# Kernel tuning notes

Hardware: AMD Instinct MI355X
Metric: run time of the kernel (lower is better)

## Reference

```python
import jax, jax.numpy as jnp
import numpy as np

BLANK = 1   # Offsets.GO
NEG = -1e30  # effective -inf that stays finite under logaddexp


def setup_inputs() -> dict:
    key = jax.random.key(0)
    k1, k2, k3, k4 = jax.random.split(key, 4)
    T, B, V, S = 1000, 64, 512, 100
    logits = jax.random.normal(k1, (T, B, V), dtype=jnp.float32)
    log_prob = jax.nn.log_softmax(logits, axis=-1)  # ctc_loss expects log-probs
    input_lengths = jax.random.randint(k2, (B,), T // 2, T + 1, dtype=jnp.int32)
    # target tokens avoid PAD(0)/GO(1,blank)/EOS(2), matching the masked_select semantics
    targets = jax.random.randint(k3, (B, S), 3, V, dtype=jnp.int32)
    target_lengths = jax.random.randint(k4, (B,), S // 2, S + 1, dtype=jnp.int32)
    return {"log_prob": log_prob, "input_lengths": input_lengths,
            "targets": targets, "target_lengths": target_lengths}


def _ctc_loss_sum(log_prob, input_lengths, targets, target_lengths):
    # log_prob: (T, B, V) log-softmax outputs; targets: (B, S) padded labels
    T, B, V = log_prob.shape
    S = targets.shape[1]
    Se = 2 * S + 1  # extended label sequence: blank-interleaved

    ext = jnp.full((B, Se), BLANK, dtype=targets.dtype).at[:, 1::2].set(targets)
    pos = jnp.arange(Se)
    ext_len = 2 * target_lengths + 1                      # (B,)
    valid = pos[None, :] < ext_len[:, None]               # (B, Se)
    ext_m2 = jnp.pad(ext[:, :-2], ((0, 0), (2, 0)), constant_values=BLANK)
    allow_skip = (ext != BLANK) & (ext != ext_m2) & (pos[None, :] >= 2)

    # emit[t, b, s] = log_prob[t, b, ext[b, s]]  -> (T, B, Se)
    emit = jnp.take_along_axis(log_prob, jnp.broadcast_to(ext[None], (T, B, Se)), axis=2)

    # alpha init at t=0
    alpha = jnp.full((B, Se), NEG, dtype=log_prob.dtype)
    alpha = alpha.at[:, 0].set(emit[0, :, 0])
    alpha = alpha.at[:, 1].set(jnp.where(target_lengths > 0, emit[0, :, 1], NEG))
    alpha = jnp.where(valid, alpha, NEG)

    def step(alpha, xt):
        emit_t, t = xt
        a1 = alpha
        a2 = jnp.pad(alpha[:, :-1], ((0, 0), (1, 0)), constant_values=NEG)
        a3 = jnp.where(allow_skip,
                       jnp.pad(alpha[:, :-2], ((0, 0), (2, 0)), constant_values=NEG),
                       NEG)
        new = jnp.logaddexp(jnp.logaddexp(a1, a2), a3) + emit_t
        new = jnp.where(valid, new, NEG)
        # freeze alpha once past each sample's input length
        alpha = jnp.where((t < input_lengths)[:, None], new, alpha)
        return alpha, None

    alpha, _ = jax.lax.scan(step, alpha, (emit[1:], jnp.arange(1, T)))

    last = 2 * target_lengths  # index of trailing blank in extended sequence
    a_last = jnp.take_along_axis(alpha, last[:, None], axis=1)[:, 0]
    a_prev = jnp.take_along_axis(alpha, jnp.maximum(last - 1, 0)[:, None], axis=1)[:, 0]
    loglik = jnp.logaddexp(a_last, a_prev)
    loss = -loglik
    # zero_infinity=True: infeasible alignments contribute 0
    loss = jnp.where(loglik < 0.5 * NEG, 0.0, loss)
    return jnp.sum(loss)  # reduction='sum'


def reference(log_prob, input_lengths, targets, target_lengths):
    return _ctc_loss_sum(log_prob, input_lengths, targets, target_lengths)
```

## Files before the change

kernel.cpp:

```cpp
#include <hip/hip_runtime.h>


#define NEGF (-1e30f)

constexpr int CT_T  = 1000;
constexpr int CT_B  = 64;
constexpr int CT_V  = 512;
constexpr int CT_S  = 100;
constexpr int CT_Se = 201;
constexpr float LOG2E = 1.4426950408889634f;
constexpr float LN2   = 0.6931471805599453f;
constexpr float SHIFT = 5.0f;

#if __has_builtin(__builtin_amdgcn_exp2f) && __has_builtin(__builtin_amdgcn_logf)
__device__ __forceinline__ float fexp2(float x) { return __builtin_amdgcn_exp2f(x); }
__device__ __forceinline__ float flog2(float x) { return __builtin_amdgcn_logf(x); }
__device__ __forceinline__ float frcp(float x)  { return __builtin_amdgcn_rcpf(x); }
#else
__device__ __forceinline__ float fexp2(float x) { return exp2f(x); }
__device__ __forceinline__ float flog2(float x) { return log2f(x); }
__device__ __forceinline__ float frcp(float x)  { return 1.0f / x; }
#endif

__device__ __forceinline__ float lae2_b2(float x, float y) {
    float m = fmaxf(x, y);
    float d = fminf(x, y) - m;
    return m + flog2(1.0f + fexp2(d));
}
__device__ __forceinline__ float lae3_b2(float x, float y, float z) {
    float m = fmaxf(fmaxf(x, y), z);
    float s = fexp2(x - m) + fexp2(y - m) + fexp2(z - m);
    return m + flog2(s);
}

__device__ __forceinline__ float wave_shr1(float x) {
    return __int_as_float(__builtin_amdgcn_update_dpp(
        0, __float_as_int(x), 0x138, 0xf, 0xf, true));
}
__device__ __forceinline__ float wave_max_nonneg(float x) {
#define DPPMAX(ctrl) x = fmaxf(x, __int_as_float(__builtin_amdgcn_update_dpp( \
        0, __float_as_int(x), ctrl, 0xf, 0xf, true)))
    DPPMAX(0x111); DPPMAX(0x112); DPPMAX(0x114); DPPMAX(0x118);
    DPPMAX(0x142); DPPMAX(0x143);
#undef DPPMAX
    return __int_as_float(__builtin_amdgcn_readlane(__float_as_int(x), 63));
}

typedef const __attribute__((address_space(1))) unsigned int* as1_uint_ptr;
typedef __attribute__((address_space(3))) unsigned int* as3_uint_ptr;
__device__ __forceinline__ void gld16(const void* g, void* l) {
    __builtin_amdgcn_global_load_lds((as1_uint_ptr)g, (as3_uint_ptr)l, 16, 0, 0);
}

__global__ __launch_bounds__(256, 1) void ctc_alpha(
    const float* __restrict__ logp,
    const int*   __restrict__ in_len,
    const int*   __restrict__ tgt,
    const int*   __restrict__ tgt_len,
    float*       __restrict__ loss_ws)
{
    __shared__ float ldsr[4][8][CT_V];

    const int b    = blockIdx.x;
    const int tid  = threadIdx.x;
    const int wv   = tid >> 6;
    const int lane = tid & 63;
    const int Tin  = in_len[b];
    const int Lt   = tgt_len[b];
    const int lim  = 2 * Lt + 1;
    const int* tg  = tgt + b * CT_S;

    const int Kf = (Tin - 1) / 8;
    const int K  = (Tin - 1 + 7) / 8;

    const int s0 = 4 * lane, s1 = s0 + 1, s3 = s0 + 3;
    const int i1 = min((s1 - 1) >> 1, CT_S - 1);
    const int i3 = min((s3 - 1) >> 1, CT_S - 1);
    const int c1 = tg[i1];
    const int c3 = tg[i3];
    const float sk1 = ((s1 >= 3) && (s1 < CT_Se) && (c1 != tg[max(i1 - 1, 0)])) ? 1.f : 0.f;
    const float sk3 = ((s3 >= 3) && (s3 < CT_Se) && (c3 != tg[max(i3 - 1, 0)])) ? 1.f : 0.f;
    const float m0 = (s0     < lim) ? 1.f : 0.f;
    const float m1 = (s0 + 1 < lim) ? 1.f : 0.f;
    const float m2 = (s0 + 2 < lim) ? 1.f : 0.f;
    const float m3 = (s0 + 3 < lim) ? 1.f : 0.f;

    float a0 = 0.f, a1 = 0.f, a2 = 0.f, a3 = 0.f, pa3 = 0.f;
    if (tid == 0) {
        const float* r0 = logp + (size_t)b * CT_V;
        a0 = fexp2(fmaf(r0[1], LOG2E, SHIFT));
        if (Lt > 0) a1 = fexp2(fmaf(r0[c1], LOG2E, SHIFT));
    }
    float rs = 0.f;

    auto issue = [&](int k, int buf) {
        const int tb = 1 + 8 * k;
        #pragma unroll
        for (int i = 0; i < 8; ++i) {
            const int t = min(tb + i, CT_T - 1);
            const char* g = (const char*)(logp + ((size_t)t * CT_B + b) * CT_V)
                          + (size_t)lane * 16;
            gld16(g,        &ldsr[buf][i][0]);
            gld16(g + 1024, &ldsr[buf][i][256]);
        }
    };

    auto renorm = [&]() {
        float lm = wave_max_nonneg(fmaxf(fmaxf(a0, a1), fmaxf(a2, a3)));
        if (lm > 0.f) {
            float sc = frcp(lm);
            rs += flog2(lm);
            a0 *= sc; a1 *= sc; a2 *= sc; a3 *= sc;
            pa3 = wave_shr1(a3);
        }
    };

    auto run8 = [&](int buf, int tb, bool guard) {
        unsigned base = (unsigned)(size_t)(&ldsr[buf][0][0]);
        unsigned ab = base + 4u * 1;
        unsigned a1a = base + 4u * (unsigned)c1;
        unsigned a3a = base + 4u * (unsigned)c3;
        float g0,g1,g2,g3,g4,g5,g6,g7,g8,g9,g10,g11,
              g12,g13,g14,g15,g16,g17,g18,g19,g20,g21,g22,g23;
        asm volatile(
            "ds_read_b32 %0,  %24 offset:0\n\t"
            "ds_read_b32 %1,  %25 offset:0\n\t"
            "ds_read_b32 %2,  %26 offset:0\n\t"
            "ds_read_b32 %3,  %24 offset:2048\n\t"
            "ds_read_b32 %4,  %25 offset:2048\n\t"
            "ds_read_b32 %5,  %26 offset:2048\n\t"
            "ds_read_b32 %6,  %24 offset:4096\n\t"
            "ds_read_b32 %7,  %25 offset:4096\n\t"
            "ds_read_b32 %8,  %26 offset:4096\n\t"
            "ds_read_b32 %9,  %24 offset:6144\n\t"
            "ds_read_b32 %10, %25 offset:6144\n\t"
            "ds_read_b32 %11, %26 offset:6144\n\t"
            "ds_read_b32 %12, %24 offset:8192\n\t"
            "ds_read_b32 %13, %25 offset:8192\n\t"
            "ds_read_b32 %14, %26 offset:8192\n\t"
            "ds_read_b32 %15, %24 offset:10240\n\t"
            "ds_read_b32 %16, %25 offset:10240\n\t"
            "ds_read_b32 %17, %26 offset:10240\n\t"
            "ds_read_b32 %18, %24 offset:12288\n\t"
            "ds_read_b32 %19, %25 offset:12288\n\t"
            "ds_read_b32 %20, %26 offset:12288\n\t"
            "ds_read_b32 %21, %24 offset:14336\n\t"
            "ds_read_b32 %22, %25 offset:14336\n\t"
            "ds_read_b32 %23, %26 offset:14336\n\t"
            "s_waitcnt lgkmcnt(0)"
            : "=&v"(g0), "=&v"(g1), "=&v"(g2), "=&v"(g3), "=&v"(g4), "=&v"(g5),
              "=&v"(g6), "=&v"(g7), "=&v"(g8), "=&v"(g9), "=&v"(g10), "=&v"(g11),
              "=&v"(g12), "=&v"(g13), "=&v"(g14), "=&v"(g15), "=&v"(g16), "=&v"(g17),
              "=&v"(g18), "=&v"(g19), "=&v"(g20), "=&v"(g21), "=&v"(g22), "=&v"(g23)
            : "v"(ab), "v"(a1a), "v"(a3a));

        float eb[8], e1[8], e3[8];
        float gb[24] = {g0,g1,g2,g3,g4,g5,g6,g7,g8,g9,g10,g11,
                        g12,g13,g14,g15,g16,g17,g18,g19,g20,g21,g22,g23};
        #pragma unroll
        for (int i = 0; i < 8; ++i) {
            eb[i] = fexp2(fmaf(gb[3 * i],     LOG2E, SHIFT));
            e1[i] = fexp2(fmaf(gb[3 * i + 1], LOG2E, SHIFT));
            e3[i] = fexp2(fmaf(gb[3 * i + 2], LOG2E, SHIFT));
        }
        #pragma unroll
        for (int i = 0; i < 8; ++i) {
            float ex = eb[i] * m0, ey = e1[i] * m1;
            float ez = eb[i] * m2, ew = e3[i] * m3;
            float n0 = (a0 + pa3) * ex;
            float n1 = fmaf(sk1, pa3, a1 + a0) * ey;
            float n2 = (a2 + a1) * ez;
            float n3 = fmaf(sk3, a1, a3 + a2) * ew;
            if (!guard || (tb + i < Tin)) { a0 = n0; a1 = n1; a2 = n2; a3 = n3; }
            pa3 = wave_shr1(a3);
        }
    };

    if (wv) {
        const int p = wv - 1;
        if (p < K) issue(p, p);
        if (p == 0)
            asm volatile("s_waitcnt vmcnt(0)" ::: "memory");
    }
    __builtin_amdgcn_s_barrier();

    for (int j = 0; j < K; ++j) {
        if (wv == 0) {
            if (j < Kf) { run8(j & 3, 0, false); if (j & 1) renorm(); }
            else        run8(j & 3, 1 + 8 * j, true);
        } else {
            const int p = wv - 1;
            if ((j % 3) == p && (j + 3) < K) issue(j + 3, (j + 3) & 3);
            if (((j + 1) % 3) == p && (j + 1) < K)
                asm volatile("s_waitcnt vmcnt(0)" ::: "memory");
        }
        __builtin_amdgcn_s_barrier();
    }

    if (wv) {
        asm volatile("s_waitcnt vmcnt(0)" ::: "memory");
        return;
    }

    const int last = 2 * Lt;
    const int prev = max(last - 1, 0);
    const int lr = last & 3, lidx = last >> 2;
    float av = (lr == 0) ? a0 : (lr == 1) ? a1 : (lr == 2) ? a2 : a3;
    float a_last = __shfl(av, lidx);
    const int pr = prev & 3, pidx = prev >> 2;
    float pv = (pr == 0) ? a0 : (pr == 1) ? a1 : (pr == 2) ? a2 : a3;
    float a_prev = __shfl(pv, pidx);

    float sum = a_last + a_prev;
    float loss = 0.f;
    if (sum > 0.f)
        loss = -(flog2(sum) + rs - SHIFT * (float)Tin) * LN2;
    if (lane == 0) loss_ws[b] = loss;
}

__global__ __launch_bounds__(64) void ctc_alpha_fb(
    const float* __restrict__ logp, const int* __restrict__ in_len,
    const int* __restrict__ tgt, const int* __restrict__ tgt_len,
    float* __restrict__ loss_ws)
{
    const int b = blockIdx.x, lane = threadIdx.x;
    const int Tin = in_len[b], Lt = tgt_len[b];
    const int ext_len = 2 * Lt + 1;
    const int* tg = tgt + b * CT_S;
    const int s0 = 4 * lane, s1 = s0 + 1, s3 = s0 + 3;
    const int i1 = min((s1 - 1) >> 1, CT_S - 1);
    const int i3 = min((s3 - 1) >> 1, CT_S - 1);
    const int c1 = tg[i1], c3 = tg[i3];
    const bool skip1 = (s1 >= 3) && (s1 < CT_Se) && (c1 != tg[max(i1 - 1, 0)]);
    const bool skip3 = (s3 >= 3) && (s3 < CT_Se) && (c3 != tg[max(i3 - 1, 0)]);
    const bool v0 = s0 < ext_len, v1 = s1 < ext_len;
    const bool v2 = (s0 + 2) < ext_len, v3 = s3 < ext_len;
    const float* row0 = logp + (long long)b * CT_V;
    const long long stride = (long long)CT_B * CT_V;
    float a0 = NEGF, a1 = NEGF, a2 = NEGF, a3 = NEGF;
    if (lane == 0) {
        a0 = row0[1] * LOG2E;
        if (ext_len > 1) a1 = row0[c1] * LOG2E;
    }
    float3 E0, E1, E2, E3;
    auto ld = [&](float3& e, int t) {
        int tt = min(t, CT_T - 1);
        const float* r = row0 + (long long)tt * stride;
        e.x = r[1] * LOG2E; e.y = r[c1] * LOG2E; e.z = r[c3] * LOG2E;
    };
    auto step = [&](const float3& e) {
        float pa3 = __shfl_up(a3, 1);
        if (lane == 0) pa3 = NEGF;
        float z1 = skip1 ? pa3 : NEGF;
        float z3 = skip3 ? a1 : NEGF;
        float n0 = v0 ? lae2_b2(a0, pa3)    + e.x : NEGF;
        float n1 = v1 ? lae3_b2(a1, a0, z1) + e.y : NEGF;
        float n2 = v2 ? lae2_b2(a2, a1)     + e.x : NEGF;
        float n3 = v3 ? lae3_b2(a3, a2, z3) + e.z : NEGF;
        a0 = n0; a1 = n1; a2 = n2; a3 = n3;
    };
    ld(E0, 1); ld(E1, 2); ld(E2, 3); ld(E3, 4);
    for (int t = 1; t < Tin; t += 4) {
        step(E0); ld(E0, t + 4);
        if (t + 1 < Tin) { step(E1); ld(E1, t + 5); }
        if (t + 2 < Tin) { step(E2); ld(E2, t + 6); }
        if (t + 3 < Tin) { step(E3); ld(E3, t + 7); }
    }
    const int last = 2 * Lt, prev = max(last - 1, 0);
    const int lr = last & 3, lidx = last >> 2;
    float av = (lr == 0) ? a0 : (lr == 1) ? a1 : (lr == 2) ? a2 : a3;
    float a_last = __shfl(av, lidx);
    const int pr = prev & 3, pidx = prev >> 2;
    float pv = (pr == 0) ? a0 : (pr == 1) ? a1 : (pr == 2) ? a2 : a3;
    float a_prev = __shfl(pv, pidx);
    float loglik = lae2_b2(a_last, a_prev) * LN2;
    float loss = (loglik < 0.5f * NEGF) ? 0.0f : -loglik;
    if (lane == 0) loss_ws[b] = loss;
}

__global__ __launch_bounds__(64) void ctc_sum(const float* __restrict__ loss_ws,
                                              float* __restrict__ out)
{
    float v = loss_ws[threadIdx.x];
    #pragma unroll
    for (int o = 32; o > 0; o >>= 1) v += __shfl_down(v, o);
    if (threadIdx.x == 0) out[0] = v;
}

extern "C" void kernel_launch(void* const* d_in, const int* in_sizes, int n_in,
                              void* d_out, int out_size, void* d_ws, size_t ws_size,
                              hipStream_t stream) {
    const float* logp    = (const float*)d_in[0];
    const int*   in_len  = (const int*)d_in[1];
    const int*   tgt     = (const int*)d_in[2];
    const int*   tgt_len = (const int*)d_in[3];
    float* out = (float*)d_out;
    float* loss_ws = (float*)d_ws;

    if (ws_size >= 256 * sizeof(float)) {
        hipLaunchKernelGGL(ctc_alpha, dim3(CT_B), dim3(256), 0, stream,
                           logp, in_len, tgt, tgt_len, loss_ws);
    } else {
        hipLaunchKernelGGL(ctc_alpha_fb, dim3(CT_B), dim3(64), 0, stream,
                           logp, in_len, tgt, tgt_len, loss_ws);
    }
    hipLaunchKernelGGL(ctc_sum, dim3(1), dim3(64), 0, stream, loss_ws, out);
}
```

Baseline: 206.1 us.

## Offload emission gather and exp2 to producer waves via compact LDS buffer

Producer waves now gather the blank and two label log-probs from the staged rows, compute exp2 on them, and write packed float4 values into a double-buffered compact LDS area. The compute wave then reads eight ds_read_b128 per chunk instead of 24 scattered ds_read_b32 and performs no transcendentals, which shortens the serial recurrence critical path. The raw staging ring drops from four buffers to three. Renorm now also runs on the final chunk. This adds LDS write traffic and makes the gather a dependency for each barrier step.

```diff
diff --git a/kernel.cpp b/kernel.cpp
--- a/kernel.cpp
+++ b/kernel.cpp
@@ -11,6 +11,8 @@
 constexpr float LOG2E = 1.4426950408889634f;
 constexpr float LN2   = 0.6931471805599453f;
 constexpr float SHIFT = 5.0f;
+
+typedef float f4 __attribute__((ext_vector_type(4)));
 
 #if __has_builtin(__builtin_amdgcn_exp2f) && __has_builtin(__builtin_amdgcn_logf)
 __device__ __forceinline__ float fexp2(float x) { return __builtin_amdgcn_exp2f(x); }
@@ -59,7 +61,8 @@
     const int*   __restrict__ tgt_len,
     float*       __restrict__ loss_ws)
 {
-    __shared__ float ldsr[4][8][CT_V];
+    __shared__ __align__(16) float sr[3][8][CT_V];
+    __shared__ __align__(16) float cp[2][8][256];
 
     const int b    = blockIdx.x;
     const int tid  = threadIdx.x;
@@ -70,8 +73,7 @@
     const int lim  = 2 * Lt + 1;
     const int* tg  = tgt + b * CT_S;
 
-    const int Kf = (Tin - 1) / 8;
-    const int K  = (Tin - 1 + 7) / 8;
+    const int K = (Tin - 1 + 7) / 8;
 
     const int s0 = 4 * lane, s1 = s0 + 1, s3 = s0 + 3;
     const int i1 = min((s1 - 1) >> 1, CT_S - 1);
@@ -93,16 +95,37 @@
     }
     float rs = 0.f;
 
-    auto issue = [&](int k, int buf) {
+    auto issue = [&](int k) {
         const int tb = 1 + 8 * k;
+        const int buf = k % 3;
         #pragma unroll
         for (int i = 0; i < 8; ++i) {
             const int t = min(tb + i, CT_T - 1);
             const char* g = (const char*)(logp + ((size_t)t * CT_B + b) * CT_V)
                           + (size_t)lane * 16;
-            gld16(g,        &ldsr[buf][i][0]);
-            gld16(g + 1024, &ldsr[buf][i][256]);
-        }
+            gld16(g,        &sr[buf][i][0]);
+            gld16(g + 1024, &sr[buf][i][256]);
+        }
+    };
+
+    auto pgather = [&](int c) {
+        asm volatile("s_waitcnt vmcnt(0)" ::: "memory");
+        __builtin_amdgcn_sched_barrier(0);
+        const int sb = c % 3, cb = c & 1;
+        #pragma unroll
+        for (int i = 0; i < 8; ++i) {
+            float gb = sr[sb][i][1];
+            float g1 = sr[sb][i][c1];
+            float g3 = sr[sb][i][c3];
+            f4 v;
+            v.x = fexp2(fmaf(gb, LOG2E, SHIFT));
+            v.y = fexp2(fmaf(g1, LOG2E, SHIFT));
+            v.z = fexp2(fmaf(g3, LOG2E, SHIFT));
+            v.w = 0.f;
+            reinterpret_cast<f4*>(&cp[cb][i][0])[lane] = v;
+        }
+        asm volatile("s_waitcnt lgkmcnt(0)" ::: "memory");
+        __builtin_amdgcn_sched_barrier(0);
     };
 
     auto renorm = [&]() {
@@ -115,58 +138,26 @@
         }
     };
 
-    auto run8 = [&](int buf, int tb, bool guard) {
-        unsigned base = (unsigned)(size_t)(&ldsr[buf][0][0]);
-        unsigned ab = base + 4u * 1;
-        unsigned a1a = base + 4u * (unsigned)c1;
-        unsigned a3a = base + 4u * (unsigned)c3;
-        float g0,g1,g2,g3,g4,g5,g6,g7,g8,g9,g10,g11,
-              g12,g13,g14,g15,g16,g17,g18,g19,g20,g21,g22,g23;
+    auto run8 = [&](int cb, int tb, bool guard) {
+        unsigned base = (unsigned)(size_t)(&cp[cb][0][0]) + 16u * (unsigned)lane;
+        f4 e[8];
         asm volatile(
-            "ds_read_b32 %0,  %24 offset:0\n\t"
-            "ds_read_b32 %1,  %25 offset:0\n\t"
-            "ds_read_b32 %2,  %26 offset:0\n\t"
-            "ds_read_b32 %3,  %24 offset:2048\n\t"
-            "ds_read_b32 %4,  %25 offset:2048\n\t"
-            "ds_read_b32 %5,  %26 offset:2048\n\t"
-            "ds_read_b32 %6,  %24 offset:4096\n\t"
-            "ds_read_b32 %7,  %25 offset:4096\n\t"
-            "ds_read_b32 %8,  %26 offset:4096\n\t"
-            "ds_read_b32 %9,  %24 offset:6144\n\t"
-            "ds_read_b32 %10, %25 offset:6144\n\t"
-            "ds_read_b32 %11, %26 offset:6144\n\t"
-            "ds_read_b32 %12, %24 offset:8192\n\t"
-            "ds_read_b32 %13, %25 offset:8192\n\t"
-            "ds_read_b32 %14, %26 offset:8192\n\t"
-            "ds_read_b32 %15, %24 offset:10240\n\t"
-            "ds_read_b32 %16, %25 offset:10240\n\t"
-            "ds_read_b32 %17, %26 offset:10240\n\t"
-            "ds_read_b32 %18, %24 offset:12288\n\t"
-            "ds_read_b32 %19, %25 offset:12288\n\t"
-            "ds_read_b32 %20, %26 offset:12288\n\t"
-            "ds_read_b32 %21, %24 offset:14336\n\t"
-            "ds_read_b32 %22, %25 offset:14336\n\t"
-            "ds_read_b32 %23, %26 offset:14336\n\t"
+            "ds_read_b128 %0, %8 offset:0\n\t"
+            "ds_read_b128 %1, %8 offset:1024\n\t"
+            "ds_read_b128 %2, %8 offset:2048\n\t"
+            "ds_read_b128 %3, %8 offset:3072\n\t"
+            "ds_read_b128 %4, %8 offset:4096\n\t"
+            "ds_read_b128 %5, %8 offset:5120\n\t"
+            "ds_read_b128 %6, %8 offset:6144\n\t"
+            "ds_read_b128 %7, %8 offset:7168\n\t"
             "s_waitcnt lgkmcnt(0)"
-            : "=&v"(g0), "=&v"(g1), "=&v"(g2), "=&v"(g3), "=&v"(g4), "=&v"(g5),
-              "=&v"(g6), "=&v"(g7), "=&v"(g8), "=&v"(g9), "=&v"(g10), "=&v"(g11),
-              "=&v"(g12), "=&v"(g13), "=&v"(g14), "=&v"(g15), "=&v"(g16), "=&v"(g17),
-              "=&v"(g18), "=&v"(g19), "=&v"(g20), "=&v"(g21), "=&v"(g22), "=&v"(g23)
-            : "v"(ab), "v"(a1a), "v"(a3a));
-
-        float eb[8], e1[8], e3[8];
-        float gb[24] = {g0,g1,g2,g3,g4,g5,g6,g7,g8,g9,g10,g11,
-                        g12,g13,g14,g15,g16,g17,g18,g19,g20,g21,g22,g23};
+            : "=&v"(e[0]), "=&v"(e[1]), "=&v"(e[2]), "=&v"(e[3]),
+              "=&v"(e[4]), "=&v"(e[5]), "=&v"(e[6]), "=&v"(e[7])
+            : "v"(base));
         #pragma unroll
         for (int i = 0; i < 8; ++i) {
-            eb[i] = fexp2(fmaf(gb[3 * i],     LOG2E, SHIFT));
-            e1[i] = fexp2(fmaf(gb[3 * i + 1], LOG2E, SHIFT));
-            e3[i] = fexp2(fmaf(gb[3 * i + 2], LOG2E, SHIFT));
-        }
-        #pragma unroll
-        for (int i = 0; i < 8; ++i) {
-            float ex = eb[i] * m0, ey = e1[i] * m1;
-            float ez = eb[i] * m2, ew = e3[i] * m3;
+            float ex = e[i].x * m0, ey = e[i].y * m1;
+            float ez = e[i].x * m2, ew = e[i].z * m3;
             float n0 = (a0 + pa3) * ex;
             float n1 = fmaf(sk1, pa3, a1 + a0) * ey;
             float n2 = (a2 + a1) * ez;
@@ -178,21 +169,19 @@
 
     if (wv) {
         const int p = wv - 1;
-        if (p < K) issue(p, p);
-        if (p == 0)
-            asm volatile("s_waitcnt vmcnt(0)" ::: "memory");
+        if (p < K) issue(p);
+        if (p == 0) pgather(0);
     }
     __builtin_amdgcn_s_barrier();
 
     for (int j = 0; j < K; ++j) {
         if (wv == 0) {
-            if (j < Kf) { run8(j & 3, 0, false); if (j & 1) renorm(); }
-            else        run8(j & 3, 1 + 8 * j, true);
+            run8(j & 1, 1 + 8 * j, j == K - 1);
+            if (j & 1) renorm();
         } else {
             const int p = wv - 1;
-            if ((j % 3) == p && (j + 3) < K) issue(j + 3, (j + 3) & 3);
-            if (((j + 1) % 3) == p && (j + 1) < K)
-                asm volatile("s_waitcnt vmcnt(0)" ::: "memory");
+            if (((j + 1) % 3) == p && (j + 1) < K) pgather(j + 1);
+            if ((j % 3) == p && (j + 3) < K) issue(j + 3);
         }
         __builtin_amdgcn_s_barrier();
     }
```

New measurement: 216.7 us. +5.1%, slower.

## Split CTC into parallel emission-precompute kernel and lean single-wave alpha recurrence

Applied to the files above, without the earlier changes.

Adds a highly parallel pre-pass that gathers the blank and label log-probs for each time step, converts them to scaled linear probabilities, and writes a compact 1 KB per (b,t) row to workspace. The alpha recurrence then runs as one wave per batch item. It streams those rows into LDS via global_load_lds with a 4-deep buffer and uses vector LDS reads, taking the gather and exp work off the serial critical path. In exchange it writes and rereads about 65 MB of workspace, adds a kernel launch, and needs a large workspace, otherwise it falls back to the old path.

```diff
diff --git a/kernel.cpp b/kernel.cpp
--- a/kernel.cpp
+++ b/kernel.cpp
@@ -11,6 +11,8 @@
 constexpr float LOG2E = 1.4426950408889634f;
 constexpr float LN2   = 0.6931471805599453f;
 constexpr float SHIFT = 5.0f;
+
+typedef float f4 __attribute__((ext_vector_type(4)));
 
 #if __has_builtin(__builtin_amdgcn_exp2f) && __has_builtin(__builtin_amdgcn_logf)
 __device__ __forceinline__ float fexp2(float x) { return __builtin_amdgcn_exp2f(x); }
@@ -52,7 +54,159 @@
     __builtin_amdgcn_global_load_lds((as1_uint_ptr)g, (as3_uint_ptr)l, 16, 0, 0);
 }
 
-__global__ __launch_bounds__(256, 1) void ctc_alpha(
+#define WAIT_VM(n) do { \
+    asm volatile("s_waitcnt vmcnt(" #n ")" ::: "memory"); \
+    __builtin_amdgcn_sched_barrier(0); } while (0)
+
+__global__ __launch_bounds__(256) void ctc_pre(
+    const float* __restrict__ logp,
+    const int*   __restrict__ tgt,
+    const int*   __restrict__ tgt_len,
+    float*       __restrict__ wsd)
+{
+    const int b    = blockIdx.x;
+    const int slab = blockIdx.y;
+    const int wv   = threadIdx.x >> 6;
+    const int lane = threadIdx.x & 63;
+    const int Lt   = tgt_len[b];
+    const int lim  = 2 * Lt + 1;
+    const int* tg  = tgt + b * CT_S;
+
+    const int s0 = 4 * lane, s1 = s0 + 1, s3 = s0 + 3;
+    const int i1 = min((s1 - 1) >> 1, CT_S - 1);
+    const int i3 = min((s3 - 1) >> 1, CT_S - 1);
+    const int c1 = tg[i1];
+    const int c3 = tg[i3];
+    const float m0 = (s0     < lim) ? 1.f : 0.f;
+    const float m1 = (s0 + 1 < lim) ? 1.f : 0.f;
+    const float m2 = (s0 + 2 < lim) ? 1.f : 0.f;
+    const float m3 = (s0 + 3 < lim) ? 1.f : 0.f;
+
+    const int t0 = slab * 125;
+    const int t1 = min(t0 + 125, CT_T);
+    for (int t = t0 + wv; t < t1; t += 4) {
+        const float* r = logp + ((size_t)t * CT_B + b) * CT_V;
+        float eb = fexp2(fmaf(r[1],  LOG2E, SHIFT));
+        float e1 = fexp2(fmaf(r[c1], LOG2E, SHIFT));
+        float e3 = fexp2(fmaf(r[c3], LOG2E, SHIFT));
+        f4 v;
+        v.x = eb * m0; v.y = e1 * m1; v.z = eb * m2; v.w = e3 * m3;
+        *reinterpret_cast<f4*>(wsd + (((size_t)b * CT_T + t) << 8) + 4 * lane) = v;
+    }
+}
+
+__global__ __launch_bounds__(64, 1) void ctc_alpha2(
+    const float* __restrict__ logp,
+    const int*   __restrict__ in_len,
+    const int*   __restrict__ tgt,
+    const int*   __restrict__ tgt_len,
+    const float* __restrict__ wsd,
+    float*       __restrict__ loss_ws)
+{
+    __shared__ __align__(16) float ldsq[4][8][256];
+
+    const int b    = blockIdx.x;
+    const int lane = threadIdx.x;
+    const int Tin  = in_len[b];
+    const int Lt   = tgt_len[b];
+    const int* tg  = tgt + b * CT_S;
+
+    const int K = (Tin - 1 + 7) / 8;
+
+    const int s1 = 4 * lane + 1, s3 = 4 * lane + 3;
+    const int i1 = min((s1 - 1) >> 1, CT_S - 1);
+    const int i3 = min((s3 - 1) >> 1, CT_S - 1);
+    const int c1 = tg[i1];
+    const float sk1 = ((s1 >= 3) && (s1 < CT_Se) && (c1 != tg[max(i1 - 1, 0)])) ? 1.f : 0.f;
+    const float sk3 = ((s3 >= 3) && (s3 < CT_Se) && (tg[i3] != tg[max(i3 - 1, 0)])) ? 1.f : 0.f;
+
+    float a0 = 0.f, a1 = 0.f, a2 = 0.f, a3 = 0.f, pa3 = 0.f;
+    if (lane == 0) {
+        const float* r0 = logp + (size_t)b * CT_V;
+        a0 = fexp2(fmaf(r0[1], LOG2E, SHIFT));
+        if (Lt > 0) a1 = fexp2(fmaf(r0[c1], LOG2E, SHIFT));
+    }
+    float rs = 0.f;
+
+    const char* src = (const char*)(wsd + ((size_t)b * CT_T << 8));
+
+    auto iss2 = [&](int k) {
+        const int tb = 1 + 8 * k;
+        const int buf = k & 3;
+        #pragma unroll
+        for (int i = 0; i < 8; ++i) {
+            const int t = min(tb + i, CT_T - 1);
+            gld16(src + ((size_t)t << 10) + (size_t)lane * 16, &ldsq[buf][i][0]);
+        }
+    };
+
+    auto renorm = [&]() {
+        float lm = wave_max_nonneg(fmaxf(fmaxf(a0, a1), fmaxf(a2, a3)));
+        if (lm > 0.f) {
+            float sc = frcp(lm);
+            rs += flog2(lm);
+            a0 *= sc; a1 *= sc; a2 *= sc; a3 *= sc;
+            pa3 = wave_shr1(a3);
+        }
+    };
+
+    auto run8 = [&](int buf, int tb, bool guard) {
+        unsigned base = (unsigned)(size_t)(&ldsq[buf][0][0]) + 16u * (unsigned)lane;
+        f4 e[8];
+        asm volatile(
+            "ds_read_b128 %0, %8 offset:0\n\t"
+            "ds_read_b128 %1, %8 offset:1024\n\t"
+            "ds_read_b128 %2, %8 offset:2048\n\t"
+            "ds_read_b128 %3, %8 offset:3072\n\t"
+            "ds_read_b128 %4, %8 offset:4096\n\t"
+            "ds_read_b128 %5, %8 offset:5120\n\t"
+            "ds_read_b128 %6, %8 offset:6144\n\t"
+            "ds_read_b128 %7, %8 offset:7168\n\t"
+            "s_waitcnt lgkmcnt(0)"
+            : "=&v"(e[0]), "=&v"(e[1]), "=&v"(e[2]), "=&v"(e[3]),
+              "=&v"(e[4]), "=&v"(e[5]), "=&v"(e[6]), "=&v"(e[7])
+            : "v"(base));
+        #pragma unroll
+        for (int i = 0; i < 8; ++i) {
+            float n0 = (a0 + pa3) * e[i].x;
+            float n1 = fmaf(sk1, pa3, a1 + a0) * e[i].y;
+            float n2 = (a2 + a1) * e[i].z;
+            float n3 = fmaf(sk3, a1, a3 + a2) * e[i].w;
+            if (!guard || (tb + i < Tin)) { a0 = n0; a1 = n1; a2 = n2; a3 = n3; }
+            pa3 = wave_shr1(a3);
+        }
+    };
+
+    WAIT_VM(0);
+    iss2(0); iss2(1); iss2(2);
+    WAIT_VM(16);
+
+    for (int j = 0; j < K; ++j) {
+        if (j + 3 < K) iss2(j + 3);
+        run8(j & 3, 1 + 8 * j, j == K - 1);
+        if (j & 1) renorm();
+        if (j + 3 < K)      { WAIT_VM(16); }
+        else if (j + 2 < K) { WAIT_VM(8); }
+        else if (j + 1 < K) { WAIT_VM(0); }
+    }
+
+    const int last = 2 * Lt;
+    const int prev = max(last - 1, 0);
+    const int lr = last & 3, lidx = last >> 2;
+    float av = (lr == 0) ? a0 : (lr == 1) ? a1 : (lr == 2) ? a2 : a3;
+    float a_last = __shfl(av, lidx);
+    const int pr = prev & 3, pidx = prev >> 2;
+    float pv = (pr == 0) ? a0 : (pr == 1) ? a1 : (pr == 2) ? a2 : a3;
+    float a_prev = __shfl(pv, pidx);
+
+    float sum = a_last + a_prev;
+    float loss = 0.f;
+    if (sum > 0.f)
+        loss = -(flog2(sum) + rs - SHIFT * (float)Tin) * LN2;
+    if (lane == 0) loss_ws[b] = loss;
+}
+
+__global__ __launch_bounds__(256, 1) void ctc_alpha_pc(
     const float* __restrict__ logp,
     const int*   __restrict__ in_len,
     const int*   __restrict__ tgt,
@@ -296,9 +450,17 @@
     const int*   tgt_len = (const int*)d_in[3];
     float* out = (float*)d_out;
     float* loss_ws = (float*)d_ws;
-
-    if (ws_size >= 256 * sizeof(float)) {
-        hipLaunchKernelGGL(ctc_alpha, dim3(CT_B), dim3(256), 0, stream,
+    float* wsd     = loss_ws + 256;
+
+    const size_t need = 1024ull + (size_t)CT_B * CT_T * 256 * 4;
+
+    if (ws_size >= need) {
+        hipLaunchKernelGGL(ctc_pre, dim3(CT_B, 8), dim3(256), 0, stream,
+                           logp, tgt, tgt_len, wsd);
+        hipLaunchKernelGGL(ctc_alpha2, dim3(CT_B), dim3(64), 0, stream,
+                           logp, in_len, tgt, tgt_len, wsd, loss_ws);
+    } else if (ws_size >= 1024) {
+        hipLaunchKernelGGL(ctc_alpha_pc, dim3(CT_B), dim3(256), 0, stream,
                            logp, in_len, tgt, tgt_len, loss_ws);
     } else {
         hipLaunchKernelGGL(ctc_alpha_fb, dim3(CT_B), dim3(64), 0, stream,
```

Result: slower. 267.9 us (+30.0%).
